# Kernel optimization log

Measured on AMD Instinct MI355X. Metric: run time of the kernel, lower is better.

## Reference

```python
import jax, jax.numpy as jnp
import numpy as np

N = 20000   # nodes per graph
E = 320000  # edges (avg degree 16)
B = 2       # batch of graphs
D = 64      # hidden_dim
L = 25      # message-passing layers
EPS = 1e-5


def setup_inputs() -> dict:
    key = jax.random.key(0)
    ks = jax.random.split(key, 12)
    rn = lambda k, s, sc=0.05: jax.random.normal(k, s, dtype=jnp.float32) * sc
    return {
        "x_batch": jax.random.normal(ks[0], (B, N, 3), dtype=jnp.float32),
        "edge_index": jax.random.randint(ks[1], (2, E), 0, N, dtype=jnp.int32),
        "edge_attr": jax.random.normal(ks[2], (E, 2), dtype=jnp.float32),
        "enc_w": rn(ks[3], (3, D)), "enc_b": jnp.zeros((D,), jnp.float32),
        "msg_w1": rn(ks[4], (L, 2 * D + 2, D)), "msg_b1": jnp.zeros((L, D), jnp.float32),
        "msg_ln_g": jnp.ones((L, D), jnp.float32), "msg_ln_b": jnp.zeros((L, D), jnp.float32),
        "msg_w2": rn(ks[5], (L, D, D)), "msg_b2": jnp.zeros((L, D), jnp.float32),
        "up_w": rn(ks[6], (L, 2 * D, D)), "up_b": jnp.zeros((L, D), jnp.float32),
        "up_ln_g": jnp.ones((L, D), jnp.float32), "up_ln_b": jnp.zeros((L, D), jnp.float32),
        "dec_w1": rn(ks[7], (D, 32)), "dec_b1": jnp.zeros((32,), jnp.float32),
        "dec_w2": rn(ks[8], (32, 2)), "dec_b2": jnp.zeros((2,), jnp.float32),
    }


def _ln(x, g, b):
    mu = jnp.mean(x, axis=-1, keepdims=True)
    var = jnp.mean(jnp.square(x - mu), axis=-1, keepdims=True)
    return (x - mu) * jax.lax.rsqrt(var + EPS) * g + b


def reference(x_batch, edge_index, edge_attr,
              enc_w, enc_b,
              msg_w1, msg_b1, msg_ln_g, msg_ln_b, msg_w2, msg_b2,
              up_w, up_b, up_ln_g, up_ln_b,
              dec_w1, dec_b1, dec_w2, dec_b2):
    row, col = edge_index[0], edge_index[1]
    layer_params = (msg_w1, msg_b1, msg_ln_g, msg_ln_b, msg_w2, msg_b2,
                    up_w, up_b, up_ln_g, up_ln_b)

    def step(h, p):  # h: [N, D]
        w1, b1, g1, be1, w2, b2, uw, ub, ug, ube = p
        cat = jnp.concatenate([h[row], h[col], edge_attr], axis=1)  # [E, 2D+2]
        m = jax.nn.relu(_ln(cat @ w1 + b1, g1, be1)) @ w2 + b2      # [E, D]
        aggr = jax.ops.segment_sum(m, row, num_segments=N)          # [N, D]
        u = jax.nn.relu(_ln(jnp.concatenate([h, aggr], axis=1) @ uw + ub, ug, ube))
        return h + u, None

    def graph(x):  # x: [N, 3]
        h0 = x @ enc_w + enc_b
        h, _ = jax.lax.scan(step, h0, layer_params)
        return jax.nn.relu(h @ dec_w1 + dec_b1) @ dec_w2 + dec_b2  # [N, 2]

    return jax.vmap(graph)(x_batch)  # [B, N, 2]
```

## Files before the change

kernel.cpp:

```cpp
#include <hip/hip_runtime.h>

constexpr int N = 20000;
constexpr int E = 320000;
constexpr int Bc = 2;
constexpr int D = 64;
constexpr int L = 25;
constexpr float EPS = 1e-5f;

typedef __attribute__((ext_vector_type(8))) short short8;
typedef __attribute__((ext_vector_type(4))) float f32x4;

__device__ __forceinline__ unsigned short f2bf(float f) {
  unsigned u = __float_as_uint(f);
  u += 0x7fff + ((u >> 16) & 1);
  return (unsigned short)(u >> 16);
}

__global__ void hist_kernel(const int* __restrict__ row, int* __restrict__ deg) {
  int e = blockIdx.x * blockDim.x + threadIdx.x;
  if (e < E) atomicAdd(&deg[row[e]], 1);
}

__global__ __launch_bounds__(1024) void scan_kernel(const int* __restrict__ deg,
                                                    int* __restrict__ row_start,
                                                    int* __restrict__ cursor) {
  __shared__ int s[1024];
  const int t = threadIdx.x;
  constexpr int CH = (N + 1023) / 1024;
  int base = t * CH;
  int sum = 0;
  for (int k = 0; k < CH; ++k) {
    int idx = base + k;
    if (idx < N) sum += deg[idx];
  }
  s[t] = sum;
  __syncthreads();
  for (int off = 1; off < 1024; off <<= 1) {
    int v = (t >= off) ? s[t - off] : 0;
    __syncthreads();
    s[t] += v;
    __syncthreads();
  }
  int excl = s[t] - sum;
  for (int k = 0; k < CH; ++k) {
    int idx = base + k;
    if (idx < N) {
      row_start[idx] = excl;
      cursor[idx] = excl;
      excl += deg[idx];
    }
  }
  if (t == 1023) row_start[N] = s[1023];
}

__global__ void scatter_kernel(const int* __restrict__ row, int* __restrict__ cursor,
                               int* __restrict__ edge_order) {
  int e = blockIdx.x * blockDim.x + threadIdx.x;
  if (e < E) {
    int p = atomicAdd(&cursor[row[e]], 1);
    edge_order[p] = e;
  }
}

__global__ void sortmap_kernel(const int* __restrict__ edge_order,
                               const int* __restrict__ col,
                               const float* __restrict__ eattr,
                               int* __restrict__ col_s, float2* __restrict__ ea_s) {
  int p = blockIdx.x * blockDim.x + threadIdx.x;
  if (p < E) {
    int eid = edge_order[p];
    col_s[p] = col[eid];
    ea_s[p] = *(const float2*)&eattr[2 * (size_t)eid];
  }
}

__global__ __launch_bounds__(512) void encoder_kernel(
    const float* __restrict__ x, const float* __restrict__ enc_w,
    const float* __restrict__ enc_b, float* __restrict__ h,
    unsigned short* __restrict__ hbf) {
  int idx = blockIdx.x * blockDim.x + threadIdx.x;
  if (idx >= Bc * N * D) return;
  int j = idx & (D - 1);
  int bn = idx >> 6;
  const float* xp = x + (size_t)bn * 3;
  float v = enc_b[j] + xp[0] * enc_w[j] + xp[1] * enc_w[D + j] + xp[2] * enc_w[2 * D + j];
  h[idx] = v;
  hbf[idx] = f2bf(v);
}

constexpr int GPN = 4;
constexpr int GPG = N / GPN;
constexpr int NGRP = GPG * Bc;
constexpr int EWB = 8;
constexpr int ETPB = EWB * 64;

__global__ __launch_bounds__(ETPB, 4) void layer_kernel(
    const unsigned short* __restrict__ hbf_old, unsigned short* __restrict__ hbf_new,
    float* __restrict__ h,
    const int* __restrict__ col_s, const float2* __restrict__ ea_s,
    const int* __restrict__ row_start,
    const float* __restrict__ w1, const float* __restrict__ b1,
    const float* __restrict__ g1, const float* __restrict__ be1,
    const float* __restrict__ w2, const float* __restrict__ b2,
    const float* __restrict__ uw, const float* __restrict__ ub,
    const float* __restrict__ ug, const float* __restrict__ ube) {
  __shared__ __align__(16) char smem[40960 + EWB * 3072];
  unsigned short* w1f = (unsigned short*)smem;
  unsigned short* w2f = (unsigned short*)(smem + 16384);
  unsigned short* uwf = (unsigned short*)(smem + 24576);

  const int tid = threadIdx.x, lane = tid & 63, w = tid >> 6;
  const int cl = lane & 15, hg = lane >> 4;
  char* pw = smem + 40960 + w * 3072;
  float* aggs = (float*)(pw + 2048);

  for (int idx = tid; idx < 16 * 512; idx += ETPB) {
    int f = idx >> 9, rem = idx & 511, ln = rem >> 3, i = rem & 7;
    int nt = f >> 2, ks = f & 3;
    int k = ks * 32 + (ln >> 4) * 8 + i, n = nt * 16 + (ln & 15);
    w1f[idx] = f2bf(w1[k * 64 + n]);
    uwf[idx] = f2bf(uw[k * 64 + n]);
  }
  for (int idx = tid; idx < 8 * 512; idx += ETPB) {
    int f = idx >> 9, rem = idx & 511, ln = rem >> 3, i = rem & 7;
    int nt = f >> 1, ks = f & 1;
    int k = ks * 32 + (ln >> 4) * 8 + i, n = nt * 16 + (ln & 15);
    w2f[idx] = f2bf(w2[k * 64 + n]);
  }
  __syncthreads();

  float b1c[4], g1c[4], be1c[4], b2c[4], wA[4], wB[4], ubc[4], ugc[4], ubec[4];
#pragma unroll
  for (int nt = 0; nt < 4; ++nt) {
    int c = nt * 16 + cl;
    b1c[nt] = b1[c]; g1c[nt] = g1[c]; be1c[nt] = be1[c]; b2c[nt] = b2[c];
    wA[nt] = w1[128 * 64 + c]; wB[nt] = w1[129 * 64 + c];
    ubc[nt] = ub[c]; ugc[nt] = ug[c]; ubec[nt] = ube[c];
  }
  const short8* w1v = (const short8*)w1f;
  const short8* w2v = (const short8*)w2f;
  const short8* uwv = (const short8*)uwf;

  const int gw = __builtin_amdgcn_readfirstlane(blockIdx.x * EWB + w);
  if (gw >= NGRP) return;
  const int g = (gw >= GPG) ? 1 : 0;
  const int nb = (gw - g * GPG) * GPN;
  const unsigned short* hb = hbf_old + (size_t)g * N * 64;

  int rs[GPN + 1];
#pragma unroll
  for (int k = 0; k <= GPN; ++k) rs[k] = row_start[nb + k];

#pragma unroll
  for (int k = 0; k < GPN; ++k) aggs[k * 64 + lane] = 0.f;

  for (int k = 0; k < GPN; ++k) {
    const int es = rs[k], ee = rs[k + 1];
    const int deg = ee - es;
    if (deg == 0) continue;
    float macc[4] = {0.f, 0.f, 0.f, 0.f};

    const unsigned short* pn = hb + (((size_t)(nb + k)) << 6) + hg * 8;
    const short8 av0 = *(const short8*)pn;
    const short8 av1 = *(const short8*)(pn + 32);

    int pos = es + cl; if (pos >= ee) pos = ee - 1;
    float2 eaC = ea_s[pos];
    const unsigned short* pc0 = hb + (((size_t)col_s[pos]) << 6) + hg * 8;
    short8 a2C = *(const short8*)pc0;
    short8 a3C = *(const short8*)(pc0 + 32);

    for (int ts = es; ts < ee; ts += 16) {
      const bool hasN = (ts + 16) < ee;
      float2 eaN; short8 a2N, a3N;
      if (hasN) {
        int p2 = ts + 16 + cl; if (p2 >= ee) p2 = ee - 1;
        eaN = ea_s[p2];
        const unsigned short* pc = hb + (((size_t)col_s[p2]) << 6) + hg * 8;
        a2N = *(const short8*)pc;
        a3N = *(const short8*)(pc + 32);
      }

      f32x4 acc[4];
#pragma unroll
      for (int nt = 0; nt < 4; ++nt) acc[nt] = (f32x4){0.f, 0.f, 0.f, 0.f};
#pragma unroll
      for (int nt = 0; nt < 4; ++nt)
        acc[nt] = __builtin_amdgcn_mfma_f32_16x16x32_bf16(av0, w1v[(nt * 4 + 0) * 64 + lane], acc[nt], 0, 0, 0);
#pragma unroll
      for (int nt = 0; nt < 4; ++nt)
        acc[nt] = __builtin_amdgcn_mfma_f32_16x16x32_bf16(av1, w1v[(nt * 4 + 1) * 64 + lane], acc[nt], 0, 0, 0);
#pragma unroll
      for (int nt = 0; nt < 4; ++nt)
        acc[nt] = __builtin_amdgcn_mfma_f32_16x16x32_bf16(a2C, w1v[(nt * 4 + 2) * 64 + lane], acc[nt], 0, 0, 0);
#pragma unroll
      for (int nt = 0; nt < 4; ++nt)
        acc[nt] = __builtin_amdgcn_mfma_f32_16x16x32_bf16(a3C, w1v[(nt * 4 + 3) * 64 + lane], acc[nt], 0, 0, 0);

#pragma unroll
      for (int r = 0; r < 4; ++r) {
        const int edge = hg * 4 + r;
        float e0 = __shfl(eaC.x, edge, 64);
        float e1 = __shfl(eaC.y, edge, 64);
        float v[4];
#pragma unroll
        for (int nt = 0; nt < 4; ++nt)
          v[nt] = acc[nt][r] + b1c[nt] + e0 * wA[nt] + e1 * wB[nt];
        float s = v[0] + v[1] + v[2] + v[3];
        float q = v[0] * v[0] + v[1] * v[1] + v[2] * v[2] + v[3] * v[3];
#pragma unroll
        for (int o = 1; o < 16; o <<= 1) {
          s += __shfl_xor(s, o, 64);
          q += __shfl_xor(q, o, 64);
        }
        float mu = s * (1.f / 64.f);
        float var = fmaf(-mu, mu, q * (1.f / 64.f));
        float rsq = rsqrtf(var + EPS);
#pragma unroll
        for (int nt = 0; nt < 4; ++nt) {
          float p = fmaxf((v[nt] - mu) * rsq * g1c[nt] + be1c[nt], 0.f);
          unsigned byteoff = (unsigned)(edge * 128 + (nt * 16 + cl) * 2) ^ (unsigned)(hg << 5);
          *(unsigned short*)(pw + byteoff) = f2bf(p);
        }
      }

      f32x4 m[4];
#pragma unroll
      for (int nt = 0; nt < 4; ++nt) m[nt] = (f32x4){0.f, 0.f, 0.f, 0.f};
#pragma unroll
      for (int ks = 0; ks < 2; ++ks) {
        unsigned byteoff = (unsigned)(cl * 128 + (ks * 32 + hg * 8) * 2) ^ (unsigned)((cl >> 2) << 5);
        short8 a2 = *(const short8*)(pw + byteoff);
#pragma unroll
        for (int nt = 0; nt < 4; ++nt)
          m[nt] = __builtin_amdgcn_mfma_f32_16x16x32_bf16(
              a2, w2v[(nt * 2 + ks) * 64 + lane], m[nt], 0, 0, 0);
      }

      const int vleft = ee - ts - hg * 4;
#pragma unroll
      for (int r = 0; r < 4; ++r) {
        if (r < vleft) {
#pragma unroll
          for (int nt = 0; nt < 4; ++nt) macc[nt] += m[nt][r];
        }
      }

      if (hasN) { eaC = eaN; a2C = a2N; a3C = a3N; }
    }

    float fin[4];
#pragma unroll
    for (int nt = 0; nt < 4; ++nt) {
      float s = macc[nt];
      s += __shfl_xor(s, 16, 64);
      s += __shfl_xor(s, 32, 64);
      fin[nt] = s + (float)deg * b2c[nt];
    }
    float sv = (hg == 0) ? fin[0] : (hg == 1) ? fin[1] : (hg == 2) ? fin[2] : fin[3];
    aggs[k * 64 + ((hg * 16 + cl) ^ (k << 3))] = sv;
  }

  {
    const int nc = (cl < GPN) ? cl : (GPN - 1);
    const unsigned short* ph = hb + (((size_t)(nb + nc)) << 6) + hg * 8;
    short8 av[4];
    av[0] = *(const short8*)ph;
    av[1] = *(const short8*)(ph + 32);
    const int i0 = nc * 64 + ((hg * 8) ^ (nc << 3));
    const int i1 = nc * 64 + (((32 + hg * 8)) ^ (nc << 3));
    float4 q0 = *(const float4*)&aggs[i0];
    float4 q1 = *(const float4*)&aggs[i0 + 4];
    float4 q2 = *(const float4*)&aggs[i1];
    float4 q3 = *(const float4*)&aggs[i1 + 4];
    {
      union { short8 s; unsigned short u[8]; } t2, t3;
      t2.u[0] = f2bf(q0.x); t2.u[1] = f2bf(q0.y); t2.u[2] = f2bf(q0.z); t2.u[3] = f2bf(q0.w);
      t2.u[4] = f2bf(q1.x); t2.u[5] = f2bf(q1.y); t2.u[6] = f2bf(q1.z); t2.u[7] = f2bf(q1.w);
      t3.u[0] = f2bf(q2.x); t3.u[1] = f2bf(q2.y); t3.u[2] = f2bf(q2.z); t3.u[3] = f2bf(q2.w);
      t3.u[4] = f2bf(q3.x); t3.u[5] = f2bf(q3.y); t3.u[6] = f2bf(q3.z); t3.u[7] = f2bf(q3.w);
      av[2] = t2.s; av[3] = t3.s;
    }

    f32x4 acc[4];
#pragma unroll
    for (int nt = 0; nt < 4; ++nt) acc[nt] = (f32x4){0.f, 0.f, 0.f, 0.f};
#pragma unroll
    for (int ks = 0; ks < 4; ++ks) {
#pragma unroll
      for (int nt = 0; nt < 4; ++nt)
        acc[nt] = __builtin_amdgcn_mfma_f32_16x16x32_bf16(
            av[ks], uwv[(nt * 4 + ks) * 64 + lane], acc[nt], 0, 0, 0);
    }

#pragma unroll
    for (int r = 0; r < 4; ++r) {
      float v[4];
#pragma unroll
      for (int nt = 0; nt < 4; ++nt) v[nt] = acc[nt][r] + ubc[nt];
      float s = v[0] + v[1] + v[2] + v[3];
      float q = v[0] * v[0] + v[1] * v[1] + v[2] * v[2] + v[3] * v[3];
#pragma unroll
      for (int o = 1; o < 16; o <<= 1) {
        s += __shfl_xor(s, o, 64);
        q += __shfl_xor(q, o, 64);
      }
      float mu = s * (1.f / 64.f);
      float var = fmaf(-mu, mu, q * (1.f / 64.f));
      float rsq = rsqrtf(var + EPS);
      if (hg == 0) {
        const size_t nrow = ((size_t)(g * N + nb + r)) << 6;
#pragma unroll
        for (int nt = 0; nt < 4; ++nt) {
          int c = nt * 16 + cl;
          float u = fmaxf((v[nt] - mu) * rsq * ugc[nt] + ubec[nt], 0.f);
          float nv = h[nrow + c] + u;
          h[nrow + c] = nv;
          hbf_new[nrow + c] = f2bf(nv);
        }
      }
    }
  }
}

__global__ __launch_bounds__(512) void decoder_kernel(
    const float* __restrict__ h,
    const float* __restrict__ dw1, const float* __restrict__ db1,
    const float* __restrict__ dw2, const float* __restrict__ db2,
    float* __restrict__ out) {
  __shared__ __align__(16) float w1s[64 * 32];
  __shared__ float w2s[64];
  __shared__ float b1s[32];
  __shared__ float hs[8][64];
  const int tid = threadIdx.x;
  const int lane = tid & 63;
  const int w = tid >> 6;

  for (int idx = tid; idx < 64 * 32; idx += 512) w1s[idx] = dw1[idx];
  if (tid < 64) w2s[tid] = dw2[tid];
  if (tid < 32) b1s[tid] = db1[tid];
  const float ob0 = db2[0], ob1 = db2[1];
  __syncthreads();

  const int total = Bc * N;
  const int per_iter = gridDim.x * 8;
  const int niter = (total + per_iter - 1) / per_iter;
  const int wave_global = blockIdx.x * 8 + w;

  for (int it = 0; it < niter; ++it) {
    const int i = it * per_iter + wave_global;
    if (i < total) {
      hs[w][lane] = h[((size_t)i << 6) + lane];
      float s1 = 0.f;
      if (lane < 32) {
        s1 = b1s[lane];
        for (int k = 0; k < 64; ++k) s1 = fmaf(hs[w][k], w1s[k * 32 + lane], s1);
        s1 = fmaxf(s1, 0.f);
      }
      float c0 = (lane < 32) ? s1 * w2s[lane * 2]     : 0.f;
      float c1 = (lane < 32) ? s1 * w2s[lane * 2 + 1] : 0.f;
#pragma unroll
      for (int off = 16; off > 0; off >>= 1) {
        c0 += __shfl_xor(c0, off, 64);
        c1 += __shfl_xor(c1, off, 64);
      }
      if (lane == 0) {
        out[(size_t)i * 2]     = c0 + ob0;
        out[(size_t)i * 2 + 1] = c1 + ob1;
      }
    }
  }
}

extern "C" void kernel_launch(void* const* d_in, const int* in_sizes, int n_in,
                              void* d_out, int out_size, void* d_ws, size_t ws_size,
                              hipStream_t stream) {
  const float* x        = (const float*)d_in[0];
  const int*   ei       = (const int*)d_in[1];
  const float* eattr    = (const float*)d_in[2];
  const float* enc_w    = (const float*)d_in[3];
  const float* enc_b    = (const float*)d_in[4];
  const float* msg_w1   = (const float*)d_in[5];
  const float* msg_b1   = (const float*)d_in[6];
  const float* msg_ln_g = (const float*)d_in[7];
  const float* msg_ln_b = (const float*)d_in[8];
  const float* msg_w2   = (const float*)d_in[9];
  const float* msg_b2   = (const float*)d_in[10];
  const float* up_w     = (const float*)d_in[11];
  const float* up_b     = (const float*)d_in[12];
  const float* up_ln_g  = (const float*)d_in[13];
  const float* up_ln_b  = (const float*)d_in[14];
  const float* dw1      = (const float*)d_in[15];
  const float* db1      = (const float*)d_in[16];
  const float* dw2      = (const float*)d_in[17];
  const float* db2      = (const float*)d_in[18];
  float* out = (float*)d_out;

  float* h             = (float*)d_ws;
  unsigned short* hbf0 = (unsigned short*)(h + (size_t)Bc * N * D);
  unsigned short* hbf1 = hbf0 + (size_t)Bc * N * D;
  float2* ea_sv        = (float2*)(hbf1 + (size_t)Bc * N * D);
  int* col_sv          = (int*)(ea_sv + E);
  int* edge_order      = col_sv + E;
  int* deg             = edge_order + E;
  int* row_start       = deg + N;
  int* cursor          = row_start + N + 1;

  const int* row = ei;
  const int* col = ei + E;

  hipMemsetAsync(deg, 0, N * sizeof(int), stream);
  hist_kernel<<<(E + 255) / 256, 256, 0, stream>>>(row, deg);
  scan_kernel<<<1, 1024, 0, stream>>>(deg, row_start, cursor);
  scatter_kernel<<<(E + 255) / 256, 256, 0, stream>>>(row, cursor, edge_order);
  sortmap_kernel<<<(E + 255) / 256, 256, 0, stream>>>(edge_order, col, eattr, col_sv, ea_sv);
  encoder_kernel<<<(Bc * N * D + 511) / 512, 512, 0, stream>>>(x, enc_w, enc_b, h, hbf0);

  unsigned short* hbufs[2] = {hbf0, hbf1};
  for (int l = 0; l < L; ++l) {
    layer_kernel<<<NGRP / EWB, ETPB, 0, stream>>>(
        hbufs[l & 1], hbufs[(l + 1) & 1], h,
        col_sv, ea_sv, row_start,
        msg_w1 + (size_t)l * 130 * 64, msg_b1 + l * 64,
        msg_ln_g + l * 64, msg_ln_b + l * 64,
        msg_w2 + (size_t)l * 64 * 64, msg_b2 + l * 64,
        up_w + (size_t)l * 128 * 64, up_b + l * 64,
        up_ln_g + l * 64, up_ln_b + l * 64);
  }

  decoder_kernel<<<512, 512, 0, stream>>>(h, dw1, db1, dw2, db2, out);
}
```

Baseline: 2.514 ms.

## Hoist w2 matmul after aggregation, prepack bf16 weights, flatten edge loop

Uses linearity to sum the relu(LN) activations per node and apply the second message matmul once per node, adding deg*b2 via an extra MFMA K row. Weights and biases for all layers are packed once into bf16 MFMA fragment layout by a new pack kernel, so layer kernels just copy them. The edge loop is flattened across the group's nodes with cross-node prefetch, and the block size is halved. Risks include extra bf16 rounding of the summed activations and global-memory reads of the w2 and update weights.

```diff
diff --git a/kernel.cpp b/kernel.cpp
--- a/kernel.cpp
+++ b/kernel.cpp
@@ -3,17 +3,26 @@
 constexpr int N = 20000;
 constexpr int E = 320000;
 constexpr int Bc = 2;
-constexpr int D = 64;
 constexpr int L = 25;
 constexpr float EPS = 1e-5f;
 
 typedef __attribute__((ext_vector_type(8))) short short8;
 typedef __attribute__((ext_vector_type(4))) float f32x4;
+typedef __attribute__((ext_vector_type(4))) unsigned short u16x4;
 
 __device__ __forceinline__ unsigned short f2bf(float f) {
   unsigned u = __float_as_uint(f);
   u += 0x7fff + ((u >> 16) & 1);
   return (unsigned short)(u >> 16);
+}
+
+__device__ __forceinline__ int sel5(int i, int a0, int a1, int a2, int a3, int a4) {
+  int r = a4;
+  r = (i == 3) ? a3 : r;
+  r = (i == 2) ? a2 : r;
+  r = (i == 1) ? a1 : r;
+  r = (i == 0) ? a0 : r;
+  return r;
 }
 
 __global__ void hist_kernel(const int* __restrict__ row, int* __restrict__ deg) {
@@ -74,16 +83,45 @@
   }
 }
 
+__global__ __launch_bounds__(512) void pack_kernel(
+    const float* __restrict__ msg_w1, const float* __restrict__ msg_b1,
+    const float* __restrict__ msg_w2, const float* __restrict__ msg_b2,
+    const float* __restrict__ up_w, const float* __restrict__ up_b,
+    unsigned short* __restrict__ wpack) {
+  const int f = blockIdx.x;
+  const int l = blockIdx.y;
+  const int t = threadIdx.x;
+  const int ln = t >> 3, i = t & 7;
+  float v = 0.f;
+  if (f < 20) {
+    int nt = f / 5, ks = f % 5;
+    int k = ks * 32 + (ln >> 4) * 8 + i, m = nt * 16 + (ln & 15);
+    if (k < 130)       v = msg_w1[(size_t)l * 130 * 64 + (size_t)k * 64 + m];
+    else if (k == 130) v = msg_b1[l * 64 + m];
+  } else if (f < 32) {
+    int f2 = f - 20, nt = f2 / 3, ks = f2 % 3;
+    int k = ks * 32 + (ln >> 4) * 8 + i, m = nt * 16 + (ln & 15);
+    if (k < 64)        v = msg_w2[(size_t)l * 64 * 64 + (size_t)k * 64 + m];
+    else if (k == 64)  v = msg_b2[l * 64 + m];
+  } else {
+    int f3 = f - 32, nt = f3 / 5, ks = f3 % 5;
+    int k = ks * 32 + (ln >> 4) * 8 + i, m = nt * 16 + (ln & 15);
+    if (k < 128)       v = up_w[(size_t)l * 128 * 64 + (size_t)k * 64 + m];
+    else if (k == 128) v = up_b[l * 64 + m];
+  }
+  wpack[((size_t)l * 52 + f) * 512 + ln * 8 + i] = f2bf(v);
+}
+
 __global__ __launch_bounds__(512) void encoder_kernel(
     const float* __restrict__ x, const float* __restrict__ enc_w,
     const float* __restrict__ enc_b, float* __restrict__ h,
     unsigned short* __restrict__ hbf) {
   int idx = blockIdx.x * blockDim.x + threadIdx.x;
-  if (idx >= Bc * N * D) return;
-  int j = idx & (D - 1);
+  if (idx >= Bc * N * 64) return;
+  int j = idx & 63;
   int bn = idx >> 6;
   const float* xp = x + (size_t)bn * 3;
-  float v = enc_b[j] + xp[0] * enc_w[j] + xp[1] * enc_w[D + j] + xp[2] * enc_w[2 * D + j];
+  float v = enc_b[j] + xp[0] * enc_w[j] + xp[1] * enc_w[64 + j] + xp[2] * enc_w[128 + j];
   h[idx] = v;
   hbf[idx] = f2bf(v);
 }
@@ -91,234 +129,282 @@
 constexpr int GPN = 4;
 constexpr int GPG = N / GPN;
 constexpr int NGRP = GPG * Bc;
-constexpr int EWB = 8;
-constexpr int ETPB = EWB * 64;
+constexpr int EWB = 4;
+constexpr int ETPB = 256;
 
 __global__ __launch_bounds__(ETPB, 4) void layer_kernel(
     const unsigned short* __restrict__ hbf_old, unsigned short* __restrict__ hbf_new,
     float* __restrict__ h,
     const int* __restrict__ col_s, const float2* __restrict__ ea_s,
     const int* __restrict__ row_start,
-    const float* __restrict__ w1, const float* __restrict__ b1,
+    const unsigned short* __restrict__ wpack_l,
     const float* __restrict__ g1, const float* __restrict__ be1,
-    const float* __restrict__ w2, const float* __restrict__ b2,
-    const float* __restrict__ uw, const float* __restrict__ ub,
     const float* __restrict__ ug, const float* __restrict__ ube) {
-  __shared__ __align__(16) char smem[40960 + EWB * 3072];
-  unsigned short* w1f = (unsigned short*)smem;
-  unsigned short* w2f = (unsigned short*)(smem + 16384);
-  unsigned short* uwf = (unsigned short*)(smem + 24576);
+  __shared__ __align__(16) unsigned short w1f[20 * 512];
+  __shared__ __align__(16) float pwb[EWB][1280];
 
   const int tid = threadIdx.x, lane = tid & 63, w = tid >> 6;
   const int cl = lane & 15, hg = lane >> 4;
-  char* pw = smem + 40960 + w * 3072;
-  float* aggs = (float*)(pw + 2048);
-
-  for (int idx = tid; idx < 16 * 512; idx += ETPB) {
-    int f = idx >> 9, rem = idx & 511, ln = rem >> 3, i = rem & 7;
-    int nt = f >> 2, ks = f & 3;
-    int k = ks * 32 + (ln >> 4) * 8 + i, n = nt * 16 + (ln & 15);
-    w1f[idx] = f2bf(w1[k * 64 + n]);
-    uwf[idx] = f2bf(uw[k * 64 + n]);
-  }
-  for (int idx = tid; idx < 8 * 512; idx += ETPB) {
-    int f = idx >> 9, rem = idx & 511, ln = rem >> 3, i = rem & 7;
-    int nt = f >> 1, ks = f & 1;
-    int k = ks * 32 + (ln >> 4) * 8 + i, n = nt * 16 + (ln & 15);
-    w2f[idx] = f2bf(w2[k * 64 + n]);
+
+  {
+    const uint4* src = (const uint4*)wpack_l;
+    uint4* dst = (uint4*)w1f;
+    for (int idx = tid; idx < 1280; idx += ETPB) dst[idx] = src[idx];
   }
   __syncthreads();
 
-  float b1c[4], g1c[4], be1c[4], b2c[4], wA[4], wB[4], ubc[4], ugc[4], ubec[4];
+  const short8* w1v = (const short8*)w1f;
+  const short8* gw2 = (const short8*)(wpack_l + 20 * 512);
+  const short8* guw = (const short8*)(wpack_l + 32 * 512);
+
+  f32x4 g1c[4], be1c[4];
 #pragma unroll
   for (int nt = 0; nt < 4; ++nt) {
-    int c = nt * 16 + cl;
-    b1c[nt] = b1[c]; g1c[nt] = g1[c]; be1c[nt] = be1[c]; b2c[nt] = b2[c];
-    wA[nt] = w1[128 * 64 + c]; wB[nt] = w1[129 * 64 + c];
-    ubc[nt] = ub[c]; ugc[nt] = ug[c]; ubec[nt] = ube[c];
-  }
-  const short8* w1v = (const short8*)w1f;
-  const short8* w2v = (const short8*)w2f;
-  const short8* uwv = (const short8*)uwf;
+    g1c[nt]  = *(const f32x4*)&g1[nt * 16 + hg * 4];
+    be1c[nt] = *(const f32x4*)&be1[nt * 16 + hg * 4];
+  }
 
   const int gw = __builtin_amdgcn_readfirstlane(blockIdx.x * EWB + w);
-  if (gw >= NGRP) return;
   const int g = (gw >= GPG) ? 1 : 0;
   const int nb = (gw - g * GPG) * GPN;
   const unsigned short* hb = hbf_old + (size_t)g * N * 64;
 
-  int rs[GPN + 1];
-#pragma unroll
-  for (int k = 0; k <= GPN; ++k) rs[k] = row_start[nb + k];
-
-#pragma unroll
-  for (int k = 0; k < GPN; ++k) aggs[k * 64 + lane] = 0.f;
-
-  for (int k = 0; k < GPN; ++k) {
-    const int es = rs[k], ee = rs[k + 1];
-    const int deg = ee - es;
-    if (deg == 0) continue;
-    float macc[4] = {0.f, 0.f, 0.f, 0.f};
-
-    const unsigned short* pn = hb + (((size_t)(nb + k)) << 6) + hg * 8;
-    const short8 av0 = *(const short8*)pn;
-    const short8 av1 = *(const short8*)(pn + 32);
-
-    int pos = es + cl; if (pos >= ee) pos = ee - 1;
-    float2 eaC = ea_s[pos];
-    const unsigned short* pc0 = hb + (((size_t)col_s[pos]) << 6) + hg * 8;
-    short8 a2C = *(const short8*)pc0;
-    short8 a3C = *(const short8*)(pc0 + 32);
-
-    for (int ts = es; ts < ee; ts += 16) {
-      const bool hasN = (ts + 16) < ee;
-      float2 eaN; short8 a2N, a3N;
-      if (hasN) {
-        int p2 = ts + 16 + cl; if (p2 >= ee) p2 = ee - 1;
-        eaN = ea_s[p2];
-        const unsigned short* pc = hb + (((size_t)col_s[p2]) << 6) + hg * 8;
-        a2N = *(const short8*)pc;
-        a3N = *(const short8*)(pc + 32);
-      }
-
-      f32x4 acc[4];
-#pragma unroll
-      for (int nt = 0; nt < 4; ++nt) acc[nt] = (f32x4){0.f, 0.f, 0.f, 0.f};
-#pragma unroll
-      for (int nt = 0; nt < 4; ++nt)
-        acc[nt] = __builtin_amdgcn_mfma_f32_16x16x32_bf16(av0, w1v[(nt * 4 + 0) * 64 + lane], acc[nt], 0, 0, 0);
-#pragma unroll
-      for (int nt = 0; nt < 4; ++nt)
-        acc[nt] = __builtin_amdgcn_mfma_f32_16x16x32_bf16(av1, w1v[(nt * 4 + 1) * 64 + lane], acc[nt], 0, 0, 0);
-#pragma unroll
-      for (int nt = 0; nt < 4; ++nt)
-        acc[nt] = __builtin_amdgcn_mfma_f32_16x16x32_bf16(a2C, w1v[(nt * 4 + 2) * 64 + lane], acc[nt], 0, 0, 0);
-#pragma unroll
-      for (int nt = 0; nt < 4; ++nt)
-        acc[nt] = __builtin_amdgcn_mfma_f32_16x16x32_bf16(a3C, w1v[(nt * 4 + 3) * 64 + lane], acc[nt], 0, 0, 0);
-
+  const int R0 = row_start[nb],     R1 = row_start[nb + 1], R2 = row_start[nb + 2],
+            R3 = row_start[nb + 3], R4 = row_start[nb + 4];
+
+  char* transB = (char*)&pwb[w][0];
+  char* aggsB  = (char*)&pwb[w][1024];
+
+#pragma unroll
+  for (int k = 0; k < 4; ++k)
+    *(float*)(aggsB + k * 256 + ((lane * 4) ^ ((k & 3) << 4))) = 0.f;
+
+  f32x4 psum[4];
+#pragma unroll
+  for (int nt = 0; nt < 4; ++nt) psum[nt] = (f32x4){0.f, 0.f, 0.f, 0.f};
+
+  auto finalize = [&](int k) {
+#pragma unroll
+    for (int nt = 0; nt < 4; ++nt)
+      *(f32x4*)(transB + cl * 256 + ((nt * 64 + hg * 16) ^ ((cl & 7) << 4))) = psum[nt];
+    float tot = 0.f;
+#pragma unroll
+    for (int e = 0; e < 16; ++e)
+      tot += *(const float*)(transB + e * 256 + ((lane * 4) ^ ((e & 7) << 4)));
+    *(float*)(aggsB + k * 256 + ((lane * 4) ^ ((k & 3) << 4))) = tot;
+#pragma unroll
+    for (int nt = 0; nt < 4; ++nt) psum[nt] = (f32x4){0.f, 0.f, 0.f, 0.f};
+  };
+
+  int kC = 0;
+  while (kC < 4 && sel5(kC + 1, R0, R1, R2, R3, R4) == sel5(kC, R0, R1, R2, R3, R4)) ++kC;
+  bool valid = (kC < 4);
+  int tsC = 0, eeC = 0;
+  short8 b2C, b3C; float2 eaC = {0.f, 0.f};
+  if (valid) {
+    tsC = sel5(kC, R0, R1, R2, R3, R4);
+    eeC = sel5(kC + 1, R0, R1, R2, R3, R4);
+    int p = tsC + cl; if (p >= eeC) p = eeC - 1;
+    const unsigned short* pc = hb + (((size_t)col_s[p]) << 6) + hg * 8;
+    b2C = *(const short8*)pc;
+    b3C = *(const short8*)(pc + 32);
+    eaC = ea_s[p];
+  }
+
+  int curk = -1;
+  f32x4 acc0[4];
+
+  while (valid) {
+    int kN = kC, tsN = tsC + 16, eeN = eeC;
+    bool validN = true;
+    if (tsN >= eeC) {
+      kN = kC + 1;
+      while (kN < 4 && sel5(kN + 1, R0, R1, R2, R3, R4) == sel5(kN, R0, R1, R2, R3, R4)) ++kN;
+      if (kN < 4) {
+        tsN = sel5(kN, R0, R1, R2, R3, R4);
+        eeN = sel5(kN + 1, R0, R1, R2, R3, R4);
+      } else validN = false;
+    }
+    short8 b2N, b3N; float2 eaN = {0.f, 0.f};
+    if (validN) {
+      int p = tsN + cl; if (p >= eeN) p = eeN - 1;
+      const unsigned short* pc = hb + (((size_t)col_s[p]) << 6) + hg * 8;
+      b2N = *(const short8*)pc;
+      b3N = *(const short8*)(pc + 32);
+      eaN = ea_s[p];
+    }
+
+    if (curk != kC) {
+      if (curk >= 0) finalize(curk);
+      curk = kC;
+      const unsigned short* pn = hb + (((size_t)(nb + kC)) << 6) + hg * 8;
+      short8 av0 = *(const short8*)pn;
+      short8 av1 = *(const short8*)(pn + 32);
+#pragma unroll
+      for (int nt = 0; nt < 4; ++nt) {
+        short8 A0 = w1v[(nt * 5 + 0) * 64 + lane];
+        short8 A1 = w1v[(nt * 5 + 1) * 64 + lane];
+        f32x4 t = __builtin_amdgcn_mfma_f32_16x16x32_bf16(A0, av0, (f32x4){0.f,0.f,0.f,0.f}, 0, 0, 0);
+        acc0[nt] = __builtin_amdgcn_mfma_f32_16x16x32_bf16(A1, av1, t, 0, 0, 0);
+      }
+    }
+
+    short8 eaB = (short8){0, 0, 0, 0, 0, 0, 0, 0};
+    if (hg == 0) {
+      eaB[0] = (short)f2bf(eaC.x);
+      eaB[1] = (short)f2bf(eaC.y);
+      eaB[2] = (short)0x3F80;
+    }
+
+    f32x4 vv[4];
+#pragma unroll
+    for (int nt = 0; nt < 4; ++nt) {
+      short8 A2 = w1v[(nt * 5 + 2) * 64 + lane];
+      short8 A3 = w1v[(nt * 5 + 3) * 64 + lane];
+      short8 A4 = w1v[(nt * 5 + 4) * 64 + lane];
+      f32x4 t = __builtin_amdgcn_mfma_f32_16x16x32_bf16(A2, b2C, acc0[nt], 0, 0, 0);
+      t = __builtin_amdgcn_mfma_f32_16x16x32_bf16(A3, b3C, t, 0, 0, 0);
+      vv[nt] = __builtin_amdgcn_mfma_f32_16x16x32_bf16(A4, eaB, t, 0, 0, 0);
+    }
+
+    float s = 0.f, q = 0.f;
+#pragma unroll
+    for (int nt = 0; nt < 4; ++nt) {
 #pragma unroll
       for (int r = 0; r < 4; ++r) {
-        const int edge = hg * 4 + r;
-        float e0 = __shfl(eaC.x, edge, 64);
-        float e1 = __shfl(eaC.y, edge, 64);
-        float v[4];
-#pragma unroll
-        for (int nt = 0; nt < 4; ++nt)
-          v[nt] = acc[nt][r] + b1c[nt] + e0 * wA[nt] + e1 * wB[nt];
-        float s = v[0] + v[1] + v[2] + v[3];
-        float q = v[0] * v[0] + v[1] * v[1] + v[2] * v[2] + v[3] * v[3];
-#pragma unroll
-        for (int o = 1; o < 16; o <<= 1) {
-          s += __shfl_xor(s, o, 64);
-          q += __shfl_xor(q, o, 64);
-        }
-        float mu = s * (1.f / 64.f);
-        float var = fmaf(-mu, mu, q * (1.f / 64.f));
-        float rsq = rsqrtf(var + EPS);
-#pragma unroll
-        for (int nt = 0; nt < 4; ++nt) {
-          float p = fmaxf((v[nt] - mu) * rsq * g1c[nt] + be1c[nt], 0.f);
-          unsigned byteoff = (unsigned)(edge * 128 + (nt * 16 + cl) * 2) ^ (unsigned)(hg << 5);
-          *(unsigned short*)(pw + byteoff) = f2bf(p);
-        }
-      }
-
-      f32x4 m[4];
-#pragma unroll
-      for (int nt = 0; nt < 4; ++nt) m[nt] = (f32x4){0.f, 0.f, 0.f, 0.f};
-#pragma unroll
-      for (int ks = 0; ks < 2; ++ks) {
-        unsigned byteoff = (unsigned)(cl * 128 + (ks * 32 + hg * 8) * 2) ^ (unsigned)((cl >> 2) << 5);
-        short8 a2 = *(const short8*)(pw + byteoff);
-#pragma unroll
-        for (int nt = 0; nt < 4; ++nt)
-          m[nt] = __builtin_amdgcn_mfma_f32_16x16x32_bf16(
-              a2, w2v[(nt * 2 + ks) * 64 + lane], m[nt], 0, 0, 0);
-      }
-
-      const int vleft = ee - ts - hg * 4;
+        s += vv[nt][r];
+        q = fmaf(vv[nt][r], vv[nt][r], q);
+      }
+    }
+    s += __shfl_xor(s, 16, 64); s += __shfl_xor(s, 32, 64);
+    q += __shfl_xor(q, 16, 64); q += __shfl_xor(q, 32, 64);
+    float mu = s * 0.015625f;
+    float var = fmaf(-mu, mu, q * 0.015625f);
+    float rsq = rsqrtf(var + EPS);
+#pragma unroll
+    for (int nt = 0; nt < 4; ++nt) {
 #pragma unroll
       for (int r = 0; r < 4; ++r) {
-        if (r < vleft) {
-#pragma unroll
-          for (int nt = 0; nt < 4; ++nt) macc[nt] += m[nt][r];
-        }
-      }
-
-      if (hasN) { eaC = eaN; a2C = a2N; a3C = a3N; }
-    }
-
-    float fin[4];
+        float gm = g1c[nt][r] * rsq;
+        vv[nt][r] = fmaxf(fmaf(vv[nt][r] - mu, gm, be1c[nt][r]), 0.f);
+      }
+    }
+
+    if (tsC + cl < eeC) {
+#pragma unroll
+      for (int nt = 0; nt < 4; ++nt) psum[nt] += vv[nt];
+    }
+
+    kC = kN; tsC = tsN; eeC = eeN; valid = validN;
+    b2C = b2N; b3C = b3N; eaC = eaN;
+  }
+  if (curk >= 0) finalize(curk);
+
+  const int n3 = (cl < 4) ? cl : 3;
+
+  short8 pB0, pB1;
+#pragma unroll
+  for (int ks = 0; ks < 2; ++ks) {
+    int x = ks * 128 + hg * 32;
+    int key = (n3 & 3) << 4;
+    f32x4 qa = *(const f32x4*)(aggsB + n3 * 256 + (x ^ key));
+    f32x4 qb = *(const f32x4*)(aggsB + n3 * 256 + ((x + 16) ^ key));
+    short8 sb;
+    sb[0] = (short)f2bf(qa[0]); sb[1] = (short)f2bf(qa[1]);
+    sb[2] = (short)f2bf(qa[2]); sb[3] = (short)f2bf(qa[3]);
+    sb[4] = (short)f2bf(qb[0]); sb[5] = (short)f2bf(qb[1]);
+    sb[6] = (short)f2bf(qb[2]); sb[7] = (short)f2bf(qb[3]);
+    if (ks == 0) pB0 = sb; else pB1 = sb;
+  }
+  float degf = 0.f;
+  if (cl == 0) degf = (float)(R1 - R0);
+  else if (cl == 1) degf = (float)(R2 - R1);
+  else if (cl == 2) degf = (float)(R3 - R2);
+  else if (cl == 3) degf = (float)(R4 - R3);
+  short8 degB = (short8){0, 0, 0, 0, 0, 0, 0, 0};
+  if (hg == 0) degB[0] = (short)f2bf(degf);
+
+  f32x4 agg[4];
+#pragma unroll
+  for (int nt = 0; nt < 4; ++nt) {
+    short8 A0 = gw2[(nt * 3 + 0) * 64 + lane];
+    short8 A1 = gw2[(nt * 3 + 1) * 64 + lane];
+    short8 A2 = gw2[(nt * 3 + 2) * 64 + lane];
+    f32x4 t = __builtin_amdgcn_mfma_f32_16x16x32_bf16(A0, pB0, (f32x4){0.f,0.f,0.f,0.f}, 0, 0, 0);
+    t = __builtin_amdgcn_mfma_f32_16x16x32_bf16(A1, pB1, t, 0, 0, 0);
+    agg[nt] = __builtin_amdgcn_mfma_f32_16x16x32_bf16(A2, degB, t, 0, 0, 0);
+  }
+
+  if (cl < 4) {
+#pragma unroll
+    for (int nt = 0; nt < 4; ++nt)
+      *(f32x4*)(transB + cl * 256 + ((nt * 64 + hg * 16) ^ ((cl & 3) << 4))) = agg[nt];
+  }
+
+  short8 uB0, uB1, uB2, uB3, uB4;
+  {
+    const unsigned short* pn = hb + (((size_t)(nb + n3)) << 6) + hg * 8;
+    uB0 = *(const short8*)pn;
+    uB1 = *(const short8*)(pn + 32);
+#pragma unroll
+    for (int ks = 0; ks < 2; ++ks) {
+      int x = ks * 128 + hg * 32;
+      int key = (n3 & 3) << 4;
+      f32x4 qa = *(const f32x4*)(transB + n3 * 256 + (x ^ key));
+      f32x4 qb = *(const f32x4*)(transB + n3 * 256 + ((x + 16) ^ key));
+      short8 sb;
+      sb[0] = (short)f2bf(qa[0]); sb[1] = (short)f2bf(qa[1]);
+      sb[2] = (short)f2bf(qa[2]); sb[3] = (short)f2bf(qa[3]);
+      sb[4] = (short)f2bf(qb[0]); sb[5] = (short)f2bf(qb[1]);
+      sb[6] = (short)f2bf(qb[2]); sb[7] = (short)f2bf(qb[3]);
+      if (ks == 0) uB2 = sb; else uB3 = sb;
+    }
+    uB4 = (short8){0, 0, 0, 0, 0, 0, 0, 0};
+    if (hg == 0) uB4[0] = (short)0x3F80;
+  }
+
+  f32x4 uacc[4];
+#pragma unroll
+  for (int nt = 0; nt < 4; ++nt) {
+    f32x4 t = __builtin_amdgcn_mfma_f32_16x16x32_bf16(guw[(nt * 5 + 0) * 64 + lane], uB0, (f32x4){0.f,0.f,0.f,0.f}, 0, 0, 0);
+    t = __builtin_amdgcn_mfma_f32_16x16x32_bf16(guw[(nt * 5 + 1) * 64 + lane], uB1, t, 0, 0, 0);
+    t = __builtin_amdgcn_mfma_f32_16x16x32_bf16(guw[(nt * 5 + 2) * 64 + lane], uB2, t, 0, 0, 0);
+    t = __builtin_amdgcn_mfma_f32_16x16x32_bf16(guw[(nt * 5 + 3) * 64 + lane], uB3, t, 0, 0, 0);
+    uacc[nt] = __builtin_amdgcn_mfma_f32_16x16x32_bf16(guw[(nt * 5 + 4) * 64 + lane], uB4, t, 0, 0, 0);
+  }
+
+  float s = 0.f, q = 0.f;
+#pragma unroll
+  for (int nt = 0; nt < 4; ++nt) {
+#pragma unroll
+    for (int r = 0; r < 4; ++r) {
+      s += uacc[nt][r];
+      q = fmaf(uacc[nt][r], uacc[nt][r], q);
+    }
+  }
+  s += __shfl_xor(s, 16, 64); s += __shfl_xor(s, 32, 64);
+  q += __shfl_xor(q, 16, 64); q += __shfl_xor(q, 32, 64);
+  float mu = s * 0.015625f;
+  float var = fmaf(-mu, mu, q * 0.015625f);
+  float rsq = rsqrtf(var + EPS);
+
+  if (cl < 4) {
+    const size_t gn = ((size_t)(g * N + nb + cl)) << 6;
 #pragma unroll
     for (int nt = 0; nt < 4; ++nt) {
-      float s = macc[nt];
-      s += __shfl_xor(s, 16, 64);
-      s += __shfl_xor(s, 32, 64);
-      fin[nt] = s + (float)deg * b2c[nt];
-    }
-    float sv = (hg == 0) ? fin[0] : (hg == 1) ? fin[1] : (hg == 2) ? fin[2] : fin[3];
-    aggs[k * 64 + ((hg * 16 + cl) ^ (k << 3))] = sv;
-  }
-
-  {
-    const int nc = (cl < GPN) ? cl : (GPN - 1);
-    const unsigned short* ph = hb + (((size_t)(nb + nc)) << 6) + hg * 8;
-    short8 av[4];
-    av[0] = *(const short8*)ph;
-    av[1] = *(const short8*)(ph + 32);
-    const int i0 = nc * 64 + ((hg * 8) ^ (nc << 3));
-    const int i1 = nc * 64 + (((32 + hg * 8)) ^ (nc << 3));
-    float4 q0 = *(const float4*)&aggs[i0];
-    float4 q1 = *(const float4*)&aggs[i0 + 4];
-    float4 q2 = *(const float4*)&aggs[i1];
-    float4 q3 = *(const float4*)&aggs[i1 + 4];
-    {
-      union { short8 s; unsigned short u[8]; } t2, t3;
-      t2.u[0] = f2bf(q0.x); t2.u[1] = f2bf(q0.y); t2.u[2] = f2bf(q0.z); t2.u[3] = f2bf(q0.w);
-      t2.u[4] = f2bf(q1.x); t2.u[5] = f2bf(q1.y); t2.u[6] = f2bf(q1.z); t2.u[7] = f2bf(q1.w);
-      t3.u[0] = f2bf(q2.x); t3.u[1] = f2bf(q2.y); t3.u[2] = f2bf(q2.z); t3.u[3] = f2bf(q2.w);
-      t3.u[4] = f2bf(q3.x); t3.u[5] = f2bf(q3.y); t3.u[6] = f2bf(q3.z); t3.u[7] = f2bf(q3.w);
-      av[2] = t2.s; av[3] = t3.s;
-    }
-
-    f32x4 acc[4];
-#pragma unroll
-    for (int nt = 0; nt < 4; ++nt) acc[nt] = (f32x4){0.f, 0.f, 0.f, 0.f};
-#pragma unroll
-    for (int ks = 0; ks < 4; ++ks) {
-#pragma unroll
-      for (int nt = 0; nt < 4; ++nt)
-        acc[nt] = __builtin_amdgcn_mfma_f32_16x16x32_bf16(
-            av[ks], uwv[(nt * 4 + ks) * 64 + lane], acc[nt], 0, 0, 0);
-    }
-
-#pragma unroll
-    for (int r = 0; r < 4; ++r) {
-      float v[4];
-#pragma unroll
-      for (int nt = 0; nt < 4; ++nt) v[nt] = acc[nt][r] + ubc[nt];
-      float s = v[0] + v[1] + v[2] + v[3];
-      float q = v[0] * v[0] + v[1] * v[1] + v[2] * v[2] + v[3] * v[3];
-#pragma unroll
-      for (int o = 1; o < 16; o <<= 1) {
-        s += __shfl_xor(s, o, 64);
-        q += __shfl_xor(q, o, 64);
-      }
-      float mu = s * (1.f / 64.f);
-      float var = fmaf(-mu, mu, q * (1.f / 64.f));
-      float rsq = rsqrtf(var + EPS);
-      if (hg == 0) {
-        const size_t nrow = ((size_t)(g * N + nb + r)) << 6;
-#pragma unroll
-        for (int nt = 0; nt < 4; ++nt) {
-          int c = nt * 16 + cl;
-          float u = fmaxf((v[nt] - mu) * rsq * ugc[nt] + ubec[nt], 0.f);
-          float nv = h[nrow + c] + u;
-          h[nrow + c] = nv;
-          hbf_new[nrow + c] = f2bf(nv);
-        }
-      }
+      f32x4 ugc  = *(const f32x4*)&ug[nt * 16 + hg * 4];
+      f32x4 ubec = *(const f32x4*)&ube[nt * 16 + hg * 4];
+      f32x4 hv = *(const f32x4*)&h[gn + nt * 16 + hg * 4];
+      u16x4 hb4;
+#pragma unroll
+      for (int r = 0; r < 4; ++r) {
+        float uu = fmaxf(fmaf(uacc[nt][r] - mu, ugc[r] * rsq, ubec[r]), 0.f);
+        float nv = hv[r] + uu;
+        hv[r] = nv;
+        hb4[r] = f2bf(nv);
+      }
+      *(f32x4*)&h[gn + nt * 16 + hg * 4] = hv;
+      *(u16x4*)&hbf_new[gn + nt * 16 + hg * 4] = hb4;
     }
   }
 }
@@ -397,9 +483,10 @@
   float* out = (float*)d_out;
 
   float* h             = (float*)d_ws;
-  unsigned short* hbf0 = (unsigned short*)(h + (size_t)Bc * N * D);
-  unsigned short* hbf1 = hbf0 + (size_t)Bc * N * D;
-  float2* ea_sv        = (float2*)(hbf1 + (size_t)Bc * N * D);
+  unsigned short* hbf0 = (unsigned short*)(h + (size_t)Bc * N * 64);
+  unsigned short* hbf1 = hbf0 + (size_t)Bc * N * 64;
+  unsigned short* wpack = hbf1 + (size_t)Bc * N * 64;
+  float2* ea_sv        = (float2*)(wpack + (size_t)L * 52 * 512);
   int* col_sv          = (int*)(ea_sv + E);
   int* edge_order      = col_sv + E;
   int* deg             = edge_order + E;
@@ -414,17 +501,17 @@
   scan_kernel<<<1, 1024, 0, stream>>>(deg, row_start, cursor);
   scatter_kernel<<<(E + 255) / 256, 256, 0, stream>>>(row, cursor, edge_order);
   sortmap_kernel<<<(E + 255) / 256, 256, 0, stream>>>(edge_order, col, eattr, col_sv, ea_sv);
-  encoder_kernel<<<(Bc * N * D + 511) / 512, 512, 0, stream>>>(x, enc_w, enc_b, h, hbf0);
+  pack_kernel<<<dim3(52, L), 512, 0, stream>>>(msg_w1, msg_b1, msg_w2, msg_b2,
+                                               up_w, up_b, wpack);
+  encoder_kernel<<<(Bc * N * 64 + 511) / 512, 512, 0, stream>>>(x, enc_w, enc_b, h, hbf0);
 
   unsigned short* hbufs[2] = {hbf0, hbf1};
   for (int l = 0; l < L; ++l) {
     layer_kernel<<<NGRP / EWB, ETPB, 0, stream>>>(
         hbufs[l & 1], hbufs[(l + 1) & 1], h,
         col_sv, ea_sv, row_start,
-        msg_w1 + (size_t)l * 130 * 64, msg_b1 + l * 64,
+        wpack + (size_t)l * 52 * 512,
         msg_ln_g + l * 64, msg_ln_b + l * 64,
-        msg_w2 + (size_t)l * 64 * 64, msg_b2 + l * 64,
-        up_w + (size_t)l * 128 * 64, up_b + l * 64,
         up_ln_g + l * 64, up_ln_b + l * 64);
   }
 
```

New measurement: 3.844 ms. 52.9% more time.
